# Kernel optimization log

Hardware: AMD Instinct MI355X
Metric: run time of the kernel (lower is better)

Reference implementation:

```python
import jax, jax.numpy as jnp
import numpy as np

N_NODES = 98304
N_EDGES = 1572864
HIDDEN = 64
N_COMM = 128


def setup_inputs() -> dict:
    key = jax.random.key(0)
    ks = jax.random.split(key, 9)
    return {
        "x_real": jax.random.normal(ks[0], (N_NODES, 1), dtype=jnp.float32),
        "x_imag": jax.random.normal(ks[1], (N_NODES, 1), dtype=jnp.float32),
        "edge_index": jax.random.randint(ks[2], (2, N_EDGES), 0, N_NODES),
        "edge_weight": jax.random.normal(ks[3], (N_EDGES,), dtype=jnp.float32),
        "comm_id": jax.random.randint(ks[4], (N_NODES,), 0, N_COMM),
        "W_local_r": jax.random.normal(ks[5], (HIDDEN, 1), dtype=jnp.float32) * 0.5,
        "W_local_i": jax.random.normal(ks[6], (HIDDEN, 1), dtype=jnp.float32) * 0.5,
        "W_global_r": jax.random.normal(ks[7], (HIDDEN, 1), dtype=jnp.float32) * 0.5,
        "W_global_i": jax.random.normal(ks[8], (HIDDEN, 1), dtype=jnp.float32) * 0.5,
    }


def reference(x_real, x_imag, edge_index, edge_weight, comm_id,
              W_local_r, W_local_i, W_global_r, W_global_i):
    """IntraInterCommunityBlock forward (combine='sum'), complex math as (real, imag) pairs.

    CommunityGNN (1 layer, no bias): complex Linear -> weighted scatter-add
    message passing -> CSiLU (SiLU applied independently to real and imag parts).
    Residual skipped because in_channels=1 != hidden (shape mismatch in source).
    Edge split by community is implemented by zero-masking edge weights, which is
    exactly equivalent for sum aggregation (message = w * x_j).
    """
    n = x_real.shape[0]
    src, dst = edge_index[0], edge_index[1]
    same = comm_id[src] == comm_id[dst]
    ew_intra = jnp.where(same, edge_weight, 0.0)
    ew_inter = jnp.where(same, 0.0, edge_weight)

    def gnn(Wr, Wi, ew):
        # complex linear: (Wr + iWi)(xr + i xi)
        hr = x_real @ Wr.T - x_imag @ Wi.T  # [N, H]
        hi = x_real @ Wi.T + x_imag @ Wr.T  # [N, H]
        # gather -> weight -> scatter-add (aggr='add')
        mr = ew[:, None] * hr[src]  # [E, H]
        mi = ew[:, None] * hi[src]
        ar = jax.ops.segment_sum(mr, dst, num_segments=n)
        ai = jax.ops.segment_sum(mi, dst, num_segments=n)
        # CSiLU: SiLU on real and imag parts
        return jax.nn.silu(ar), jax.nn.silu(ai)

    lr, li = gnn(W_local_r, W_local_i, ew_intra)
    gr, gi = gnn(W_global_r, W_global_i, ew_inter)
    # combine='sum'; stack real/imag on last axis -> [N, H, 2]
    return jnp.stack([lr + gr, li + gi], axis=-1)
```

## Files before the change

kernel.cpp:

```cpp
#include <hip/hip_runtime.h>

#define N_NODES 98304
#define N_EDGES 1572864
#define HIDDEN  64

#define NB      384
#define CAP     4608
#define NBLK    384
#define CHUNK   4096
#define TPB_S   512
#define EPT_S   8
#define SEG     4

#define FP_SCALE 1048576.0f
#define FP_INV   (1.0f / 1048576.0f)

__device__ __forceinline__ float silu_f(float x) {
    return x / (1.0f + __expf(-x));
}


__global__ __launch_bounds__(TPB_S) void scatter_kernel(const int* __restrict__ ei,
    const float* __restrict__ ew,
    const float* __restrict__ xr,
    const float* __restrict__ xi,
    const int* __restrict__ comm,
    unsigned* __restrict__ ctr,
    unsigned long long* __restrict__ payload)
{
    __shared__ unsigned long long sorted[CHUNK];
    __shared__ unsigned short bucketOf[CHUNK];
    __shared__ unsigned hist[NB];
    __shared__ unsigned localbase[NB];
    __shared__ unsigned baseS[NB];

    const int tid = threadIdx.x, blk = blockIdx.x;
    for (int i = tid; i < NB; i += TPB_S) hist[i] = 0;
    __syncthreads();

    const int ebase = blk * CHUNK;
    unsigned long long pay[EPT_S];
    unsigned pb[EPT_S], pr[EPT_S];
#pragma unroll
    for (int k = 0; k < EPT_S; ++k) {
        const int e = ebase + k * TPB_S + tid;
        const int s = ei[e];
        const int d = ei[N_EDGES + e];
        const float w = ew[e];
        const float vr = xr[s];
        const float vi = xi[s];
        const int dr = __float2int_rn(w * vr * FP_SCALE);
        const int di = __float2int_rn(w * vi * FP_SCALE);
        const unsigned flag = (comm[s] == comm[d]) ? 0u : 1u;
        const unsigned b = (unsigned)d >> 8;
        pb[k] = b;
        pr[k] = atomicAdd(&hist[b], 1u);
        pay[k] = ((unsigned long long)((unsigned)dr & 0x07FFFFFFu) << 37)
               | ((unsigned long long)((unsigned)di & 0x07FFFFFFu) << 10)
               | ((unsigned)(d & 255) << 2) | ((unsigned long long)flag << 1);
    }
    __syncthreads();

    if (tid < 64) {
        unsigned v[6];
        unsigned s = 0;
#pragma unroll
        for (int m = 0; m < 6; ++m) { v[m] = hist[tid * 6 + m]; s += v[m]; }
        unsigned p = s;
#pragma unroll
        for (int off = 1; off < 64; off <<= 1) {
            unsigned t = __shfl_up(p, off);
            if (tid >= off) p += t;
        }
        unsigned excl = p - s;
#pragma unroll
        for (int m = 0; m < 6; ++m) { unsigned t = v[m]; localbase[tid * 6 + m] = excl; excl += t; }
    }
    __syncthreads();

    for (int i = tid; i < NB; i += TPB_S)
        baseS[i] = (unsigned)i * CAP + atomicAdd(&ctr[i], hist[i]);
#pragma unroll
    for (int k = 0; k < EPT_S; ++k) {
        const unsigned pos = localbase[pb[k]] + pr[k];
        sorted[pos] = pay[k];
        bucketOf[pos] = (unsigned short)pb[k];
    }
    __syncthreads();

    for (int i = tid; i < CHUNK; i += TPB_S) {
        const unsigned b = bucketOf[i];
        const unsigned slot = baseS[b] + ((unsigned)i - localbase[b]);
        if (slot < ((unsigned)b + 1u) * CAP)
            payload[slot] = sorted[i];
    }
}

__global__ __launch_bounds__(256) void accum_epilogue_kernel(
    const unsigned long long* __restrict__ payload,
    const unsigned* __restrict__ ctr,
    const float* __restrict__ Wlr, const float* __restrict__ Wli,
    const float* __restrict__ Wgr, const float* __restrict__ Wgi,
    float4* __restrict__ out)
{
    __shared__ int accR[128];
    __shared__ int accI[128];
    __shared__ float2 w_s[4][32];
    const int tid = threadIdx.x;
    const int x    = blockIdx.x & 7;
    const int slot = blockIdx.x >> 3;
    const int bucket = x * (NB / 8) + (slot >> 2);
    const int seg    = slot & 3;

    if (tid < 128) { accR[tid] = 0; accI[tid] = 0; }
    else {
        const int t = tid - 128;
        const int which = t >> 5, h2 = t & 31;
        const float* W = (which == 0) ? Wlr : (which == 1) ? Wli
                       : (which == 2) ? Wgr : Wgi;
        w_s[which][h2] = ((const float2*)W)[h2];
    }
    __syncthreads();

    unsigned cnt = ctr[bucket];
    if (cnt > CAP) cnt = CAP;
    const unsigned long long* buck = payload + (size_t)bucket * CAP;
    for (unsigned i = tid; i < cnt; i += 256) {
        const unsigned long long p = buck[i];
        const unsigned ln = (unsigned)(p >> 2) & 255u;
        if ((int)(ln >> 6) == seg) {
            const int dr = (int)((long long)p >> 37);
            const int di = (int)(((long long)(p << 27)) >> 37);
            const unsigned idx = ((ln & 63u) << 1) | ((unsigned)(p >> 1) & 1u);
            atomicAdd(&accR[idx], dr);
            atomicAdd(&accI[idx], di);
        }
    }
    __syncthreads();

#pragma unroll
    for (int j = 0; j < 8; ++j) {
        const int idx = j * 256 + tid;
        const int ln  = idx >> 5;
        const int h2  = idx & 31;
        const float sr_l = (float)accR[ln * 2 + 0] * FP_INV;
        const float si_l = (float)accI[ln * 2 + 0] * FP_INV;
        const float sr_g = (float)accR[ln * 2 + 1] * FP_INV;
        const float si_g = (float)accI[ln * 2 + 1] * FP_INV;
        const float2 a = w_s[0][h2], c = w_s[1][h2];
        const float2 g = w_s[2][h2], f = w_s[3][h2];
        float4 o;
        {
            const float arl = a.x * sr_l - c.x * si_l;
            const float ail = c.x * sr_l + a.x * si_l;
            const float arg = g.x * sr_g - f.x * si_g;
            const float aig = f.x * sr_g + g.x * si_g;
            o.x = silu_f(arl) + silu_f(arg);
            o.y = silu_f(ail) + silu_f(aig);
        }
        {
            const float arl = a.y * sr_l - c.y * si_l;
            const float ail = c.y * sr_l + a.y * si_l;
            const float arg = g.y * sr_g - f.y * si_g;
            const float aig = f.y * sr_g + g.y * si_g;
            o.z = silu_f(arl) + silu_f(arg);
            o.w = silu_f(ail) + silu_f(aig);
        }
        out[(size_t)bucket * 8192 + (size_t)seg * 2048 + idx] = o;
    }
}


#define FB_SCALE 2097152.0f
#define FB_INV   (1.0f / 2097152.0f)

__global__ void edge_scatter_fb(const int* __restrict__ ei,
                                const float* __restrict__ ew,
                                const int* __restrict__ comm,
                                const float* __restrict__ xr,
                                const float* __restrict__ xi,
                                unsigned long long* __restrict__ P)
{
    const int e = blockIdx.x * blockDim.x + threadIdx.x;
    if (e >= N_EDGES) return;
    const int s = ei[e];
    const int d = ei[N_EDGES + e];
    const float w = ew[e];
    const int dr = __float2int_rn(w * xr[s] * FB_SCALE);
    const int di = __float2int_rn(w * xi[s] * FB_SCALE);
    const unsigned long long delta =
        (unsigned long long)(((long long)dr << 32) + (long long)di);
    const int base = (comm[s] == comm[d]) ? 0 : N_NODES;
    atomicAdd(&P[base + d], delta);
}

__global__ void epilogue_fb(const unsigned long long* __restrict__ P,
                            const float* __restrict__ Wlr,
                            const float* __restrict__ Wli,
                            const float* __restrict__ Wgr,
                            const float* __restrict__ Wgi,
                            float4* __restrict__ out)
{
    const int total = N_NODES * (HIDDEN / 2);
    const int t = blockIdx.x * blockDim.x + threadIdx.x;
    if (t >= total) return;
    const int n = t >> 5, h2 = t & 31;
    float sr_l, si_l, sr_g, si_g;
    {
        const unsigned long long U = P[n];
        const int bi = (int)(unsigned)(U & 0xffffffffULL);
        const int ar = (int)(unsigned)(U >> 32) + (bi < 0 ? 1 : 0);
        sr_l = (float)ar * FB_INV; si_l = (float)bi * FB_INV;
    }
    {
        const unsigned long long U = P[N_NODES + n];
        const int bi = (int)(unsigned)(U & 0xffffffffULL);
        const int ar = (int)(unsigned)(U >> 32) + (bi < 0 ? 1 : 0);
        sr_g = (float)ar * FB_INV; si_g = (float)bi * FB_INV;
    }
    const float2 wlr = ((const float2*)Wlr)[h2];
    const float2 wli = ((const float2*)Wli)[h2];
    const float2 wgr = ((const float2*)Wgr)[h2];
    const float2 wgi = ((const float2*)Wgi)[h2];
    float4 o;
    {
        const float arl = wlr.x * sr_l - wli.x * si_l;
        const float ail = wli.x * sr_l + wlr.x * si_l;
        const float arg = wgr.x * sr_g - wgi.x * si_g;
        const float aig = wgi.x * sr_g + wgr.x * si_g;
        o.x = silu_f(arl) + silu_f(arg);
        o.y = silu_f(ail) + silu_f(aig);
    }
    {
        const float arl = wlr.y * sr_l - wli.y * si_l;
        const float ail = wli.y * sr_l + wlr.y * si_l;
        const float arg = wgr.y * sr_g - wgi.y * si_g;
        const float aig = wgi.y * sr_g + wgr.y * si_g;
        o.z = silu_f(arl) + silu_f(arg);
        o.w = silu_f(ail) + silu_f(aig);
    }
    out[t] = o;
}

extern "C" void kernel_launch(void* const* d_in, const int* in_sizes, int n_in,
                              void* d_out, int out_size, void* d_ws, size_t ws_size,
                              hipStream_t stream) {
    const float* xr   = (const float*)d_in[0];
    const float* xi   = (const float*)d_in[1];
    const int*   ei   = (const int*)d_in[2];
    const float* ew   = (const float*)d_in[3];
    const int*   comm = (const int*)d_in[4];
    const float* Wlr  = (const float*)d_in[5];
    const float* Wli  = (const float*)d_in[6];
    const float* Wgr  = (const float*)d_in[7];
    const float* Wgi  = (const float*)d_in[8];

    const size_t payload_bytes = (size_t)NB * CAP * sizeof(unsigned long long);
    const size_t ctr_bytes     = 4096;
    const size_t need = payload_bytes + ctr_bytes;

    if (ws_size >= need) {
        char* p = (char*)d_ws;
        unsigned long long* payload = (unsigned long long*)p;  p += payload_bytes;
        unsigned* ctr               = (unsigned*)p;

        hipMemsetAsync(ctr, 0, NB * sizeof(unsigned), stream);
        hipLaunchKernelGGL(scatter_kernel, dim3(NBLK), dim3(TPB_S), 0, stream,
                           ei, ew, xr, xi, comm, ctr, payload);
        hipLaunchKernelGGL(accum_epilogue_kernel, dim3(NB * SEG), dim3(256), 0, stream,
                           payload, ctr, Wlr, Wli, Wgr, Wgi, (float4*)d_out);
    } else {
        unsigned long long* P = (unsigned long long*)d_ws;
        hipMemsetAsync(P, 0, (size_t)2 * N_NODES * sizeof(unsigned long long), stream);
        hipLaunchKernelGGL(edge_scatter_fb, dim3((N_EDGES + 255) / 256), dim3(256), 0, stream,
                           ei, ew, comm, xr, xi, P);
        const int total = N_NODES * (HIDDEN / 2);
        hipLaunchKernelGGL(epilogue_fb, dim3((total + 255) / 256), dim3(256), 0, stream,
                           P, Wlr, Wli, Wgr, Wgi, (float4*)d_out);
    }
}
```

Measured before the change: 70.47 us.

## Replace global bucket counters with per-chunk sorted payload and offset table

```diff
diff --git a/kernel.cpp b/kernel.cpp
--- a/kernel.cpp
+++ b/kernel.cpp
@@ -5,52 +5,45 @@
 #define HIDDEN  64
 
 #define NB      384
-#define CAP     4608
-#define NBLK    384
-#define CHUNK   4096
-#define TPB_S   512
-#define EPT_S   8
-#define SEG     4
+#define NBLK    1536
+#define CHUNK   1024
+#define TPB     256
+#define EPT     4
+#define NBX     (NB / 8)
 
 #define FP_SCALE 1048576.0f
 #define FP_INV   (1.0f / 1048576.0f)
 
+typedef float float4n __attribute__((ext_vector_type(4)));
+
 __device__ __forceinline__ float silu_f(float x) {
     return x / (1.0f + __expf(-x));
 }
 
-
-__global__ __launch_bounds__(TPB_S) void scatter_kernel(const int* __restrict__ ei,
-    const float* __restrict__ ew,
-    const float* __restrict__ xr,
-    const float* __restrict__ xi,
-    const int* __restrict__ comm,
-    unsigned* __restrict__ ctr,
-    unsigned long long* __restrict__ payload)
+__global__ __launch_bounds__(TPB) void k_scatter(const int* __restrict__ ei,
+    const float* __restrict__ ew, const float* __restrict__ xr,
+    const float* __restrict__ xi, const int* __restrict__ comm,
+    unsigned short* __restrict__ lbT, unsigned long long* __restrict__ payload)
 {
     __shared__ unsigned long long sorted[CHUNK];
-    __shared__ unsigned short bucketOf[CHUNK];
     __shared__ unsigned hist[NB];
     __shared__ unsigned localbase[NB];
-    __shared__ unsigned baseS[NB];
 
     const int tid = threadIdx.x, blk = blockIdx.x;
-    for (int i = tid; i < NB; i += TPB_S) hist[i] = 0;
+    for (int i = tid; i < NB; i += TPB) hist[i] = 0;
     __syncthreads();
 
     const int ebase = blk * CHUNK;
-    unsigned long long pay[EPT_S];
-    unsigned pb[EPT_S], pr[EPT_S];
-#pragma unroll
-    for (int k = 0; k < EPT_S; ++k) {
-        const int e = ebase + k * TPB_S + tid;
-        const int s = ei[e];
-        const int d = ei[N_EDGES + e];
-        const float w = ew[e];
-        const float vr = xr[s];
-        const float vi = xi[s];
-        const int dr = __float2int_rn(w * vr * FP_SCALE);
-        const int di = __float2int_rn(w * vi * FP_SCALE);
+    unsigned long long pay[EPT];
+    unsigned pb[EPT], pr[EPT];
+#pragma unroll
+    for (int k = 0; k < EPT; ++k) {
+        const int e = ebase + k * TPB + tid;
+        const int s = __builtin_nontemporal_load(&ei[e]);
+        const int d = __builtin_nontemporal_load(&ei[N_EDGES + e]);
+        const float w = __builtin_nontemporal_load(&ew[e]);
+        const int dr = __float2int_rn(w * xr[s] * FP_SCALE);
+        const int di = __float2int_rn(w * xi[s] * FP_SCALE);
         const unsigned flag = (comm[s] == comm[d]) ? 0u : 1u;
         const unsigned b = (unsigned)d >> 8;
         pb[k] = b;
@@ -78,39 +71,35 @@
     }
     __syncthreads();
 
-    for (int i = tid; i < NB; i += TPB_S)
-        baseS[i] = (unsigned)i * CAP + atomicAdd(&ctr[i], hist[i]);
-#pragma unroll
-    for (int k = 0; k < EPT_S; ++k) {
-        const unsigned pos = localbase[pb[k]] + pr[k];
-        sorted[pos] = pay[k];
-        bucketOf[pos] = (unsigned short)pb[k];
-    }
-    __syncthreads();
-
-    for (int i = tid; i < CHUNK; i += TPB_S) {
-        const unsigned b = bucketOf[i];
-        const unsigned slot = baseS[b] + ((unsigned)i - localbase[b]);
-        if (slot < ((unsigned)b + 1u) * CAP)
-            payload[slot] = sorted[i];
-    }
-}
-
-__global__ __launch_bounds__(256) void accum_epilogue_kernel(
+#pragma unroll
+    for (int k = 0; k < EPT; ++k)
+        sorted[localbase[pb[k]] + pr[k]] = pay[k];
+    for (int i = tid; i < NB; i += TPB)
+        lbT[(size_t)blk * NB + i] = (unsigned short)localbase[i];
+    __syncthreads();
+
+    const ulonglong2* src2 = (const ulonglong2*)sorted;
+    ulonglong2* dst2 = (ulonglong2*)(payload + (size_t)blk * CHUNK);
+#pragma unroll
+    for (int i = tid; i < CHUNK / 2; i += TPB)
+        dst2[i] = src2[i];
+}
+
+__global__ __launch_bounds__(TPB) void k_accum_final(
     const unsigned long long* __restrict__ payload,
-    const unsigned* __restrict__ ctr,
+    const unsigned short* __restrict__ lbT,
     const float* __restrict__ Wlr, const float* __restrict__ Wli,
     const float* __restrict__ Wgr, const float* __restrict__ Wgi,
-    float4* __restrict__ out)
+    float* __restrict__ out)
 {
     __shared__ int accR[128];
     __shared__ int accI[128];
     __shared__ float2 w_s[4][32];
-    const int tid = threadIdx.x;
-    const int x    = blockIdx.x & 7;
-    const int slot = blockIdx.x >> 3;
-    const int bucket = x * (NB / 8) + (slot >> 2);
-    const int seg    = slot & 3;
+    const int tid = threadIdx.x, blk = blockIdx.x;
+    const int xcd = blk & 7;
+    const int j   = blk >> 3;
+    const int bucket = xcd * NBX + (j >> 2);
+    const int seg    = j & 3;
 
     if (tid < 128) { accR[tid] = 0; accI[tid] = 0; }
     else {
@@ -122,25 +111,31 @@
     }
     __syncthreads();
 
-    unsigned cnt = ctr[bucket];
-    if (cnt > CAP) cnt = CAP;
-    const unsigned long long* buck = payload + (size_t)bucket * CAP;
-    for (unsigned i = tid; i < cnt; i += 256) {
-        const unsigned long long p = buck[i];
-        const unsigned ln = (unsigned)(p >> 2) & 255u;
-        if ((int)(ln >> 6) == seg) {
-            const int dr = (int)((long long)p >> 37);
-            const int di = (int)(((long long)(p << 27)) >> 37);
-            const unsigned idx = ((ln & 63u) << 1) | ((unsigned)(p >> 1) & 1u);
-            atomicAdd(&accR[idx], dr);
-            atomicAdd(&accI[idx], di);
-        }
-    }
-    __syncthreads();
-
-#pragma unroll
-    for (int j = 0; j < 8; ++j) {
-        const int idx = j * 256 + tid;
+    for (int c = tid; c < NBLK; c += TPB) {
+        const unsigned base = lbT[(size_t)c * NB + bucket];
+        const unsigned next = (bucket < NB - 1)
+                            ? (unsigned)lbT[(size_t)c * NB + bucket + 1]
+                            : (unsigned)CHUNK;
+        const unsigned long long* chunkp = payload + (size_t)c * CHUNK;
+        for (unsigned i = base; i < next; ++i) {
+            const unsigned long long p = chunkp[i];
+            const unsigned ln = (unsigned)(p >> 2) & 255u;
+            if ((int)(ln >> 6) == seg) {
+                const int dr = (int)((long long)p >> 37);
+                const int di = (int)(((long long)(p << 27)) >> 37);
+                const unsigned idx = ((ln & 63u) << 1) | ((unsigned)(p >> 1) & 1u);
+                atomicAdd(&accR[idx], dr);
+                atomicAdd(&accI[idx], di);
+            }
+        }
+    }
+    __syncthreads();
+
+    float4n* outv = (float4n*)out;
+    const size_t obase = (size_t)bucket * 8192 + (size_t)seg * 2048;
+#pragma unroll
+    for (int jj = 0; jj < 8; ++jj) {
+        const int idx = jj * 256 + tid;
         const int ln  = idx >> 5;
         const int h2  = idx & 31;
         const float sr_l = (float)accR[ln * 2 + 0] * FP_INV;
@@ -149,7 +144,7 @@
         const float si_g = (float)accI[ln * 2 + 1] * FP_INV;
         const float2 a = w_s[0][h2], c = w_s[1][h2];
         const float2 g = w_s[2][h2], f = w_s[3][h2];
-        float4 o;
+        float4n o;
         {
             const float arl = a.x * sr_l - c.x * si_l;
             const float ail = c.x * sr_l + a.x * si_l;
@@ -166,13 +161,9 @@
             o.z = silu_f(arl) + silu_f(arg);
             o.w = silu_f(ail) + silu_f(aig);
         }
-        out[(size_t)bucket * 8192 + (size_t)seg * 2048 + idx] = o;
-    }
-}
-
-
-#define FB_SCALE 2097152.0f
-#define FB_INV   (1.0f / 2097152.0f)
+        __builtin_nontemporal_store(o, &outv[obase + idx]);
+    }
+}
 
 __global__ void edge_scatter_fb(const int* __restrict__ ei,
                                 const float* __restrict__ ew,
@@ -186,8 +177,8 @@
     const int s = ei[e];
     const int d = ei[N_EDGES + e];
     const float w = ew[e];
-    const int dr = __float2int_rn(w * xr[s] * FB_SCALE);
-    const int di = __float2int_rn(w * xi[s] * FB_SCALE);
+    const int dr = __float2int_rn(w * xr[s] * FP_SCALE);
+    const int di = __float2int_rn(w * xi[s] * FP_SCALE);
     const unsigned long long delta =
         (unsigned long long)(((long long)dr << 32) + (long long)di);
     const int base = (comm[s] == comm[d]) ? 0 : N_NODES;
@@ -210,13 +201,13 @@
         const unsigned long long U = P[n];
         const int bi = (int)(unsigned)(U & 0xffffffffULL);
         const int ar = (int)(unsigned)(U >> 32) + (bi < 0 ? 1 : 0);
-        sr_l = (float)ar * FB_INV; si_l = (float)bi * FB_INV;
+        sr_l = (float)ar * FP_INV; si_l = (float)bi * FP_INV;
     }
     {
         const unsigned long long U = P[N_NODES + n];
         const int bi = (int)(unsigned)(U & 0xffffffffULL);
         const int ar = (int)(unsigned)(U >> 32) + (bi < 0 ? 1 : 0);
-        sr_g = (float)ar * FB_INV; si_g = (float)bi * FB_INV;
+        sr_g = (float)ar * FP_INV; si_g = (float)bi * FP_INV;
     }
     const float2 wlr = ((const float2*)Wlr)[h2];
     const float2 wli = ((const float2*)Wli)[h2];
@@ -255,20 +246,19 @@
     const float* Wgr  = (const float*)d_in[7];
     const float* Wgi  = (const float*)d_in[8];
 
-    const size_t payload_bytes = (size_t)NB * CAP * sizeof(unsigned long long);
-    const size_t ctr_bytes     = 4096;
-    const size_t need = payload_bytes + ctr_bytes;
+    const size_t payload_bytes = (size_t)N_EDGES * sizeof(unsigned long long);
+    const size_t lbT_bytes     = (size_t)NBLK * NB * sizeof(unsigned short);
+    const size_t need = payload_bytes + lbT_bytes;
 
     if (ws_size >= need) {
         char* p = (char*)d_ws;
         unsigned long long* payload = (unsigned long long*)p;  p += payload_bytes;
-        unsigned* ctr               = (unsigned*)p;
-
-        hipMemsetAsync(ctr, 0, NB * sizeof(unsigned), stream);
-        hipLaunchKernelGGL(scatter_kernel, dim3(NBLK), dim3(TPB_S), 0, stream,
-                           ei, ew, xr, xi, comm, ctr, payload);
-        hipLaunchKernelGGL(accum_epilogue_kernel, dim3(NB * SEG), dim3(256), 0, stream,
-                           payload, ctr, Wlr, Wli, Wgr, Wgi, (float4*)d_out);
+        unsigned short* lbT         = (unsigned short*)p;
+
+        hipLaunchKernelGGL(k_scatter, dim3(NBLK), dim3(TPB), 0, stream,
+                           ei, ew, xr, xi, comm, lbT, payload);
+        hipLaunchKernelGGL(k_accum_final, dim3(NBLK), dim3(TPB), 0, stream,
+                           payload, lbT, Wlr, Wli, Wgr, Wgi, (float*)d_out);
     } else {
         unsigned long long* P = (unsigned long long*)d_ws;
         hipMemsetAsync(P, 0, (size_t)2 * N_NODES * sizeof(unsigned long long), stream);
```

Result: slower. 91.74 us (+30.2%).
